# Kernel optimization log

Measured on AMD Instinct MI355X. Metric: run time of the kernel, lower is better.

## Reference

```python
import jax, jax.numpy as jnp
import numpy as np

N = 10000
F_IN, F_HID, F_OUT = 128, 64, 32
E = 320000
MAX_LOGSTD = 10.0


def _glorot(key, fan_in, fan_out):
    lim = np.sqrt(6.0 / (fan_in + fan_out))
    return jax.random.uniform(key, (fan_in, fan_out), jnp.float32, -lim, lim)


def setup_inputs() -> dict:
    key = jax.random.key(0)
    ks = jax.random.split(key, 8)
    x = jax.random.normal(ks[0], (N, F_IN), jnp.float32)
    edge_index = jax.random.randint(ks[1], (2, E), 0, N, jnp.int64)
    eps = jax.random.normal(ks[2], (N, F_OUT), jnp.float32)
    return {
        'x': x,
        'edge_index': edge_index,
        'eps': eps,
        'W0': _glorot(ks[3], F_IN, F_HID), 'b0': jnp.zeros((F_HID,), jnp.float32),
        'W1': _glorot(ks[4], F_HID, F_HID), 'b1': jnp.zeros((F_HID,), jnp.float32),
        'Wmu': _glorot(ks[5], F_HID, F_OUT), 'bmu': jnp.zeros((F_OUT,), jnp.float32),
        'Wls': _glorot(ks[6], F_HID, F_OUT), 'bls': jnp.zeros((F_OUT,), jnp.float32),
    }


def _gcn_norm(edge_index, n):
    # add self-loops, symmetric normalization (PyG gcn_norm, improved=False)
    loop = jnp.arange(n, dtype=edge_index.dtype)
    src = jnp.concatenate([edge_index[0], loop])
    dst = jnp.concatenate([edge_index[1], loop])
    deg = jax.ops.segment_sum(jnp.ones_like(src, jnp.float32), dst, num_segments=n)
    dinv = jnp.where(deg > 0, deg ** -0.5, 0.0)
    norm = dinv[src] * dinv[dst]  # [E+N]
    return src, dst, norm


def _gcn_conv(x, W, b, src, dst, norm, n):
    h = x @ W                              # [N, Fo] dense transform
    m = norm[:, None] * h[src]             # per-edge gather + scale
    return jax.ops.segment_sum(m, dst, num_segments=n) + b  # scatter-add


def reference(x, edge_index, eps, W0, b0, W1, b1, Wmu, bmu, Wls, bls):
    n = x.shape[0]
    src, dst, norm = _gcn_norm(edge_index, n)
    h = jax.nn.relu(_gcn_conv(x, W0, b0, src, dst, norm, n))
    h = jax.nn.relu(_gcn_conv(h, W1, b1, src, dst, norm, n))
    mu = _gcn_conv(h, Wmu, bmu, src, dst, norm, n)
    logstd = jnp.minimum(_gcn_conv(h, Wls, bls, src, dst, norm, n), MAX_LOGSTD)
    z = mu + eps * jnp.exp(logstd)         # VGAE reparameterize (training mode)
    adj_pred = jax.nn.sigmoid(z @ z.T)     # InnerProductDecoder.forward_all
    return adj_pred
```

## Files before the change

kernel.cpp:

```cpp
#include <hip/hip_runtime.h>
#include <math.h>

#define FIN 128

typedef float f32x4 __attribute__((ext_vector_type(4)));


__global__ void k_count(const int* __restrict__ dst, int* __restrict__ deg, int E) {
    int e = blockIdx.x * blockDim.x + threadIdx.x;
    if (e < E) atomicAdd(&deg[dst[e]], 1);
}

__global__ __launch_bounds__(256) void k_prescan(const int* __restrict__ deg,
                                                 int* __restrict__ boff,
                                                 int* __restrict__ rowptr, int n) {
    __shared__ int bs[64];
    int NB = (n + 255) >> 8;
    int c = threadIdx.x;
    if (c < 64) {
        int s = 0;
        if (c < NB) {
            int base = c << 8;
            int lim = n - base; if (lim > 256) lim = 256;
            for (int i = 0; i < lim; ++i) s += deg[base + i];
        }
        bs[c] = s;
    }
    __syncthreads();
    if (threadIdx.x < 64) {
        int v = bs[threadIdx.x];
        int incl = v;
        for (int off = 1; off < 64; off <<= 1) {
            int o = __shfl_up(incl, off);
            if ((int)threadIdx.x >= off) incl += o;
        }
        if ((int)threadIdx.x < NB) boff[threadIdx.x] = incl - v;
        if (threadIdx.x == 63) rowptr[n] = incl;
    }
}

__global__ __launch_bounds__(256) void k_scatter(const int* __restrict__ deg,
                                                 const int* __restrict__ boff,
                                                 int* __restrict__ rowptr,
                                                 float* __restrict__ dinv, int n) {
    __shared__ int buf[256];
    int i = blockIdx.x * 256 + threadIdx.x;
    int v = (i < n) ? deg[i] : 0;
    if (i < n) dinv[i] = rsqrtf((float)v + 1.0f);
    buf[threadIdx.x] = v;
    __syncthreads();
    for (int off = 1; off < 256; off <<= 1) {
        int o = (threadIdx.x >= off) ? buf[threadIdx.x - off] : 0;
        __syncthreads();
        buf[threadIdx.x] += o;
        __syncthreads();
    }
    if (i < n) rowptr[i] = boff[blockIdx.x] + buf[threadIdx.x] - v;
}

__global__ void k_fill(const int* __restrict__ src, const int* __restrict__ dst,
                       const float* __restrict__ dinv, const int* __restrict__ rowptr,
                       int* __restrict__ fillcnt, int2* __restrict__ csr, int E) {
    int e = blockIdx.x * blockDim.x + threadIdx.x;
    if (e >= E) return;
    int s = src[e], d = dst[e];
    float w = dinv[s] * dinv[d];
    int pos = rowptr[d] + atomicAdd(&fillcnt[d], 1);
    csr[pos] = make_int2(s, __float_as_int(w));
}


template<int K, int CAT>
__global__ __launch_bounds__(256) void k_xform(const float* __restrict__ in,
                                               const float* __restrict__ Wa,
                                               const float* __restrict__ Wb,
                                               float* __restrict__ out, int n) {
    __shared__ float Ws[K * 64];
    if (CAT) {
        for (int i = threadIdx.x; i < 64 * 64; i += 256) {
            int k = i >> 6, j = i & 63;
            Ws[i] = (j < 32) ? Wa[k * 32 + j] : Wb[k * 32 + (j - 32)];
        }
    } else {
        for (int i = threadIdx.x; i < K * 64; i += 256) Ws[i] = Wa[i];
    }
    __syncthreads();
    int lane = threadIdx.x & 63;
    int wv = threadIdx.x >> 6;
#pragma unroll
    for (int r = 0; r < 4; ++r) {
        int row = blockIdx.x * 16 + wv * 4 + r;
        if (row >= n) continue;
        const float* xr = in + (long long)row * K;
        float xa = xr[lane];
        float xb = (K > 64) ? xr[(K > 64 ? 64 : 0) + lane] : 0.0f;
        float acc = 0.0f;
#pragma unroll
        for (int k = 0; k < K; ++k) {
            float xk = (k < 64) ? __shfl(xa, k) : __shfl(xb, k - 64);
            acc += xk * Ws[k * 64 + lane];
        }
        out[(long long)row * 64 + lane] = acc;
    }
}


template<int MODE>
__global__ __launch_bounds__(256) void k_prop(const float* __restrict__ t,
                                              const int2* __restrict__ csr,
                                              const int* __restrict__ rowptr,
                                              const float* __restrict__ dinv,
                                              const float* __restrict__ ba,
                                              const float* __restrict__ bb,
                                              const float* __restrict__ eps,
                                              float* __restrict__ out, int n) {
    int lane = threadIdx.x & 63;
    int node = blockIdx.x * 4 + (threadIdx.x >> 6);
    if (node >= n) return;
    float di = dinv[node];
    float acc = di * di * t[(long long)node * 64 + lane];
    int e0 = rowptr[node], e1 = rowptr[node + 1];
    for (int base = e0; base < e1; base += 64) {
        int m = e1 - base; if (m > 64) m = 64;
        int2 my = make_int2(0, 0);
        if (lane < m) my = csr[base + lane];
        for (int i = 0; i < m; ++i) {
            int s = __shfl(my.x, i);
            float w = __int_as_float(__shfl(my.y, i));
            acc += w * t[(long long)s * 64 + lane];
        }
    }
    if (MODE == 0) {
        out[(long long)node * 64 + lane] = fmaxf(acc + ba[lane], 0.0f);
    } else {
        float v = acc + ((lane < 32) ? ba[lane] : bb[lane - 32]);
        float ls = __shfl(v, lane | 32);
        if (lane < 32) {
            float zv = v + eps[(long long)node * 32 + lane] * __expf(fminf(ls, 10.0f));
            out[(long long)node * 32 + lane] = zv;
        }
    }
}


__global__ __launch_bounds__(256) void k_decoder(const float* __restrict__ z,
                                                 float* __restrict__ out, int n) {
    __shared__ float ziT[32][132];
    __shared__ float zjT[32][132];
    int i0 = blockIdx.y * 128;
    int j0 = blockIdx.x * 128;
    int t = threadIdx.x;
#pragma unroll
    for (int r = 0; r < 4; ++r) {
        int idx = t + r * 256;
        int row = idx >> 3;
        int c4 = (idx & 7) << 2;
        float4 vi = make_float4(0.f, 0.f, 0.f, 0.f);
        float4 vj = make_float4(0.f, 0.f, 0.f, 0.f);
        if (i0 + row < n) vi = *(const float4*)&z[(long long)(i0 + row) * 32 + c4];
        if (j0 + row < n) vj = *(const float4*)&z[(long long)(j0 + row) * 32 + c4];
        ziT[c4 + 0][row] = vi.x; ziT[c4 + 1][row] = vi.y;
        ziT[c4 + 2][row] = vi.z; ziT[c4 + 3][row] = vi.w;
        zjT[c4 + 0][row] = vj.x; zjT[c4 + 1][row] = vj.y;
        zjT[c4 + 2][row] = vj.z; zjT[c4 + 3][row] = vj.w;
    }
    __syncthreads();

    int tr = t >> 4, tc = t & 15;
    int rbase = tr * 8, cbase = tc * 8;
    float acc[8][8];
#pragma unroll
    for (int u = 0; u < 8; ++u)
#pragma unroll
        for (int v = 0; v < 8; ++v) acc[u][v] = 0.0f;

#pragma unroll 4
    for (int k = 0; k < 32; ++k) {
        float4 a0 = *(const float4*)&ziT[k][rbase];
        float4 a1 = *(const float4*)&ziT[k][rbase + 4];
        float4 b0v = *(const float4*)&zjT[k][cbase];
        float4 b1v = *(const float4*)&zjT[k][cbase + 4];
        float a[8] = {a0.x, a0.y, a0.z, a0.w, a1.x, a1.y, a1.z, a1.w};
        float b[8] = {b0v.x, b0v.y, b0v.z, b0v.w, b1v.x, b1v.y, b1v.z, b1v.w};
#pragma unroll
        for (int u = 0; u < 8; ++u)
#pragma unroll
            for (int v = 0; v < 8; ++v)
                acc[u][v] += a[u] * b[v];
    }

#pragma unroll
    for (int u = 0; u < 8; ++u) {
        int gi = i0 + rbase + u;
        if (gi < n) {
            float r[8];
#pragma unroll
            for (int v = 0; v < 8; ++v)
                r[v] = __fdividef(1.0f, 1.0f + __expf(-acc[u][v]));
            long long base = (long long)gi * n + (j0 + cbase);
            if (j0 + cbase + 8 <= n) {
                *(float4*)&out[base]     = make_float4(r[0], r[1], r[2], r[3]);
                *(float4*)&out[base + 4] = make_float4(r[4], r[5], r[6], r[7]);
            } else {
#pragma unroll
                for (int v = 0; v < 8; ++v)
                    if (j0 + cbase + v < n) out[base + v] = r[v];
            }
        }
    }
}


extern "C" void kernel_launch(void* const* d_in, const int* in_sizes, int n_in,
                              void* d_out, int out_size, void* d_ws, size_t ws_size,
                              hipStream_t stream) {
    const float* x   = (const float*)d_in[0];
    const int*   ei  = (const int*)d_in[1];
    const float* eps = (const float*)d_in[2];
    const float* W0  = (const float*)d_in[3];
    const float* b0  = (const float*)d_in[4];
    const float* W1  = (const float*)d_in[5];
    const float* b1  = (const float*)d_in[6];
    const float* Wmu = (const float*)d_in[7];
    const float* bmu = (const float*)d_in[8];
    const float* Wls = (const float*)d_in[9];
    const float* bls = (const float*)d_in[10];
    float* out = (float*)d_out;

    int E = in_sizes[1] / 2;
    int n = in_sizes[0] / FIN;

    char* ws = (char*)d_ws;
    int*   deg     = (int*)(ws + 0);
    int*   fillcnt = (int*)(ws + 40960);
    int*   boff    = (int*)(ws + 81920);
    int*   rowptr  = (int*)(ws + 82432);
    float* dinv    = (float*)(ws + 124928);
    int2*  csr     = (int2*)(ws + 165888);
    float* bufA    = (float*)(ws + 2725888);
    float* bufB    = (float*)(ws + 5285888);
    float* z       = (float*)(ws + 7845888);

    const int* src = ei;
    const int* dst = ei + E;

    (void)hipMemsetAsync(deg, 0, 81920, stream);
    k_count<<<(E + 255) / 256, 256, 0, stream>>>(dst, deg, E);
    k_prescan<<<1, 256, 0, stream>>>(deg, boff, rowptr, n);
    int nb = (n + 255) / 256;
    k_scatter<<<nb, 256, 0, stream>>>(deg, boff, rowptr, dinv, n);
    k_fill<<<(E + 255) / 256, 256, 0, stream>>>(src, dst, dinv, rowptr, fillcnt, csr, E);

    int xblocks = (n + 15) / 16;
    int pblocks = (n + 3) / 4;
    k_xform<128, 0><<<xblocks, 256, 0, stream>>>(x, W0, nullptr, bufA, n);
    k_prop<0><<<pblocks, 256, 0, stream>>>(bufA, csr, rowptr, dinv, b0, nullptr, nullptr, bufB, n);
    k_xform<64, 0><<<xblocks, 256, 0, stream>>>(bufB, W1, nullptr, bufA, n);
    k_prop<0><<<pblocks, 256, 0, stream>>>(bufA, csr, rowptr, dinv, b1, nullptr, nullptr, bufB, n);
    k_xform<64, 1><<<xblocks, 256, 0, stream>>>(bufB, Wmu, Wls, bufA, n);
    k_prop<1><<<pblocks, 256, 0, stream>>>(bufA, csr, rowptr, dinv, bmu, bls, eps, z, n);

    int nt = (n + 127) / 128;
    dim3 g(nt, nt);
    k_decoder<<<g, 256, 0, stream>>>(z, out, n);
}
```

Before: 650.3 us.

## Exploit symmetry of z·zᵀ by computing upper-triangle tiles and mirroring

The decoder now launches only upper-triangular 128x128 tiles and writes each off-diagonal tile twice: directly, and transposed through shared memory into the mirrored position. This roughly halves the dot-product and sigmoid work and the z tile loads. The output write volume is unchanged, and that dominates a 10000x10000 float store. In exchange it adds a serial loop that maps block index to tile, plus extra syncthreads and shared-memory staging for the transposed stores.

Result: slower. 693.2 us (+6.6%).

```diff
diff --git a/kernel.cpp b/kernel.cpp
--- a/kernel.cpp
+++ b/kernel.cpp
@@ -144,12 +144,19 @@
 
 
 __global__ __launch_bounds__(256) void k_decoder(const float* __restrict__ z,
-                                                 float* __restrict__ out, int n) {
-    __shared__ float ziT[32][132];
-    __shared__ float zjT[32][132];
-    int i0 = blockIdx.y * 128;
-    int j0 = blockIdx.x * 128;
+                                                 float* __restrict__ out,
+                                                 int n, int nt) {
+    __shared__ float smem[2 * 32 * 132];
+    float* ziT = smem;
+    float* zjT = smem + 32 * 132;
+
+    int bid = blockIdx.x;
+    int bi = 0, rem = nt;
+    while (bid >= rem) { bid -= rem; ++bi; --rem; }
+    int bj = bi + bid;
+    int i0 = bi * 128, j0 = bj * 128;
     int t = threadIdx.x;
+
 #pragma unroll
     for (int r = 0; r < 4; ++r) {
         int idx = t + r * 256;
@@ -159,10 +166,10 @@
         float4 vj = make_float4(0.f, 0.f, 0.f, 0.f);
         if (i0 + row < n) vi = *(const float4*)&z[(long long)(i0 + row) * 32 + c4];
         if (j0 + row < n) vj = *(const float4*)&z[(long long)(j0 + row) * 32 + c4];
-        ziT[c4 + 0][row] = vi.x; ziT[c4 + 1][row] = vi.y;
-        ziT[c4 + 2][row] = vi.z; ziT[c4 + 3][row] = vi.w;
-        zjT[c4 + 0][row] = vj.x; zjT[c4 + 1][row] = vj.y;
-        zjT[c4 + 2][row] = vj.z; zjT[c4 + 3][row] = vj.w;
+        ziT[(c4 + 0) * 132 + row] = vi.x; ziT[(c4 + 1) * 132 + row] = vi.y;
+        ziT[(c4 + 2) * 132 + row] = vi.z; ziT[(c4 + 3) * 132 + row] = vi.w;
+        zjT[(c4 + 0) * 132 + row] = vj.x; zjT[(c4 + 1) * 132 + row] = vj.y;
+        zjT[(c4 + 2) * 132 + row] = vj.z; zjT[(c4 + 3) * 132 + row] = vj.w;
     }
     __syncthreads();
 
@@ -176,10 +183,10 @@
 
 #pragma unroll 4
     for (int k = 0; k < 32; ++k) {
-        float4 a0 = *(const float4*)&ziT[k][rbase];
-        float4 a1 = *(const float4*)&ziT[k][rbase + 4];
-        float4 b0v = *(const float4*)&zjT[k][cbase];
-        float4 b1v = *(const float4*)&zjT[k][cbase + 4];
+        float4 a0 = *(const float4*)&ziT[k * 132 + rbase];
+        float4 a1 = *(const float4*)&ziT[k * 132 + rbase + 4];
+        float4 b0v = *(const float4*)&zjT[k * 132 + cbase];
+        float4 b1v = *(const float4*)&zjT[k * 132 + cbase + 4];
         float a[8] = {a0.x, a0.y, a0.z, a0.w, a1.x, a1.y, a1.z, a1.w};
         float b[8] = {b0v.x, b0v.y, b0v.z, b0v.w, b1v.x, b1v.y, b1v.z, b1v.w};
 #pragma unroll
@@ -205,6 +212,41 @@
 #pragma unroll
                 for (int v = 0; v < 8; ++v)
                     if (j0 + cbase + v < n) out[base + v] = r[v];
+            }
+        }
+    }
+
+    if (bi != bj) {
+        float* Ltr = smem;
+#pragma unroll
+        for (int p = 0; p < 4; ++p) {
+            __syncthreads();
+            if ((tc >> 2) == p) {
+#pragma unroll
+                for (int v = 0; v < 8; ++v) {
+                    int cl = (tc & 3) * 8 + v;
+#pragma unroll
+                    for (int u = 0; u < 8; ++u)
+                        Ltr[cl * 132 + rbase + u] =
+                            __fdividef(1.0f, 1.0f + __expf(-acc[u][v]));
+                }
+            }
+            __syncthreads();
+            int mrl = t >> 3;
+            int mc0 = (t & 7) * 16;
+            int gr = j0 + p * 32 + mrl;
+            if (gr < n) {
+                long long ob = (long long)gr * n + i0 + mc0;
+                if (i0 + mc0 + 16 <= n) {
+#pragma unroll
+                    for (int q = 0; q < 4; ++q)
+                        *(float4*)&out[ob + q * 4] =
+                            *(const float4*)&Ltr[mrl * 132 + mc0 + q * 4];
+                } else {
+#pragma unroll
+                    for (int e = 0; e < 16; ++e)
+                        if (i0 + mc0 + e < n) out[ob + e] = Ltr[mrl * 132 + mc0 + e];
+                }
             }
         }
     }
@@ -261,6 +303,6 @@
     k_prop<1><<<pblocks, 256, 0, stream>>>(bufA, csr, rowptr, dinv, bmu, bls, eps, z, n);
 
     int nt = (n + 127) / 128;
-    dim3 g(nt, nt);
-    k_decoder<<<g, 256, 0, stream>>>(z, out, n);
-}
+    int nblk = nt * (nt + 1) / 2;
+    k_decoder<<<nblk, 256, 0, stream>>>(z, out, n, nt);
+}
```
